# Performance work log

Hardware: AMD Instinct MI355X
Metric: run time of the kernel (lower is better)

## Reference

```python
import jax, jax.numpy as jnp
import numpy as np

B, H, M, K = 256, 1024, 20, 20  # batch, hidden, max_ingr, pairing top_k (must be equal: M==K)
VOCAB, INGR_V = 32000, 5000


def setup_inputs() -> dict:
    key = jax.random.key(0)
    ks = jax.random.split(key, 24)
    s = 0.02
    inp = {
        "input_ids": jax.random.randint(ks[0], (1, B), 0, VOCAB),
        "hidden": jax.random.normal(ks[1], (1, B, H), jnp.float32),
        "encoder_outputs": jax.random.normal(ks[2], (M, B, 2 * H), jnp.float32),
        "input_tensor": jax.random.randint(ks[3], (B, M), 0, INGR_V),
        "pairing_ids": jax.random.randint(ks[4], (INGR_V, K), 0, INGR_V),
        # parameters
        "emb_dec": jax.random.normal(ks[5], (VOCAB, H), jnp.float32) * s,
        "enc_emb": jax.random.normal(ks[6], (INGR_V, 2 * H), jnp.float32) * s,
        "Wq_i": jax.random.normal(ks[7], (H, H), jnp.float32) * s,
        "Wk_i": jax.random.normal(ks[8], (2 * H, H), jnp.float32) * s,
        "wa_i": jax.random.normal(ks[9], (H,), jnp.float32) * s,
        "Wq_p": jax.random.normal(ks[10], (H, H), jnp.float32) * s,
        "Wk_p": jax.random.normal(ks[11], (2 * H, H), jnp.float32) * s,
        "wa_p": jax.random.normal(ks[12], (H,), jnp.float32) * s,
        "ba_p": jax.random.normal(ks[13], (), jnp.float32) * s,
        "W_lin": jax.random.normal(ks[14], (3 * H, 2 * H), jnp.float32) * s,
        "b_lin": jnp.zeros((2 * H,), jnp.float32),
        "W_ih": jax.random.normal(ks[15], (3 * H, 2 * H), jnp.float32) * s,
        "W_hh": jax.random.normal(ks[16], (3 * H, H), jnp.float32) * s,
        "b_ih": jnp.zeros((3 * H,), jnp.float32),
        "b_hh": jnp.zeros((3 * H,), jnp.float32),
        "W_out": jax.random.normal(ks[17], (H, VOCAB), jnp.float32) * s,
        "b_out": jnp.zeros((VOCAB,), jnp.float32),
    }
    return inp


def reference(input_ids, hidden, encoder_outputs, input_tensor, pairing_ids,
              emb_dec, enc_emb, Wq_i, Wk_i, wa_i, Wq_p, Wk_p, wa_p, ba_p,
              W_lin, b_lin, W_ih, W_hh, b_ih, b_hh, W_out, b_out):
    h = hidden[0]                              # (B, H)
    emb = jnp.take(emb_dec, input_ids[0], axis=0)  # (B, H)

    # ---- IngrAtt (additive attention over ingredients) ----
    # torch code does a raw .view(B, M, 2H) on a (M, B, 2H) tensor -> plain reshape
    enc = encoder_outputs.reshape(B, M, 2 * H)
    query = h @ Wq_i                           # (B, H)
    key = enc @ Wk_i                           # (B, M, H)
    scores_i = jnp.tanh(query[:, None, :] + key) @ wa_i  # (B, M)
    aw = jax.nn.softmax(scores_i, axis=-1)     # (B, M)

    # ---- retrieval: pick most-attended ingredient, gather its top-k pairings ----
    ingr_arg = jnp.argmax(aw, axis=1)                          # (B,)
    ingr_id = input_tensor[jnp.arange(B), ingr_arg]            # (B,)
    comp_ids = jnp.take(pairing_ids, ingr_id, axis=0)          # (B, K)
    comp_emb = jnp.take(enc_emb, comp_ids, axis=0)             # (B, K, 2H)

    # ---- PairingAtt ----
    q_p = h @ Wq_p                             # (B, H)
    k_p = comp_emb @ Wk_p                      # (B, K, H)
    s_p = jnp.tanh(q_p[:, None, :] + k_p) @ wa_p + ba_p  # (B, K)
    a_p = jax.nn.softmax(s_p, axis=-1)
    attn_scores = a_p * s_p                    # (B, K) softmax-weighted raw scores
    attn_app = jnp.einsum('bk,bkd->bd', attn_scores, comp_emb)  # (B, 2H)

    out_pair = jnp.concatenate([emb, attn_app], axis=-1)  # (B, 3H)
    x = out_pair @ W_lin + b_lin                           # (B, 2H) -> GRU input

    # ---- single GRU step (torch gate ordering r,z,n) ----
    gi = x @ W_ih.T + b_ih
    gh = h @ W_hh.T + b_hh
    i_r, i_z, i_n = jnp.split(gi, 3, axis=-1)
    h_r, h_z, h_n = jnp.split(gh, 3, axis=-1)
    r = jax.nn.sigmoid(i_r + h_r)
    z = jax.nn.sigmoid(i_z + h_z)
    n = jnp.tanh(i_n + r * h_n)
    h_new = (1.0 - z) * n + z * h              # (B, H)

    logits = h_new @ W_out + b_out             # (B, VOCAB)
    return logits
```

## Files before the change

kernel.cpp:

```cpp
#include <hip/hip_runtime.h>
#include <cstdio>


using f32x4   = __attribute__((ext_vector_type(4))) float;
using bf16x8  = __attribute__((ext_vector_type(8))) short;
using ushort8 = __attribute__((ext_vector_type(8))) unsigned short;

__device__ __forceinline__ unsigned short f2bf(float x) {
    unsigned u = __builtin_bit_cast(unsigned, x);
    u += 0x7fffu + ((u >> 16) & 1u);
    return (unsigned short)(u >> 16);
}
__device__ __forceinline__ float bf2f(unsigned short u) {
    return __builtin_bit_cast(float, ((unsigned)u) << 16);
}

__device__ __forceinline__ void gload16(const void* g, void* l) {
    auto gp = (const __attribute__((address_space(1))) void*)g;
    auto lp = (__attribute__((address_space(3))) void*)l;
    __builtin_amdgcn_global_load_lds(gp, lp, 16, 0, 0);
}

__device__ __forceinline__ void transpose_body(
    const float* __restrict__ in, unsigned short* __restrict__ out,
    int R, int C, int r0, int c0)
{
    __shared__ float t[32][129];
    const int tid = threadIdx.x;
    const int lr = tid >> 3;
    const int cc = (tid & 7) * 4;
    #pragma unroll
    for (int i = 0; i < 4; ++i) {
        int r = lr + 32 * i;
        float4 v = *(const float4*)(in + (size_t)(r0 + r) * C + c0 + cc);
        t[cc + 0][r] = v.x; t[cc + 1][r] = v.y;
        t[cc + 2][r] = v.z; t[cc + 3][r] = v.w;
    }
    __syncthreads();
    const int rc = (tid & 15) * 8;
    #pragma unroll
    for (int p = 0; p < 2; ++p) {
        int c = (tid >> 4) + 16 * p;
        const float* src = &t[c][rc];
        ushort8 o;
        #pragma unroll
        for (int j = 0; j < 8; ++j) o[j] = f2bf(src[j]);
        *(ushort8*)(out + (size_t)(c0 + c) * R + r0 + rc) = o;
    }
}

__global__ __launch_bounds__(256) void prep1_kernel(
    const float* __restrict__ hidden, const float* __restrict__ enc_out,
    const float* __restrict__ enc_emb,
    const float* __restrict__ Wq_i, const float* __restrict__ Wq_p,
    const float* __restrict__ Wk_i, const float* __restrict__ Wk_p,
    unsigned short* __restrict__ hb, unsigned short* __restrict__ encb,
    unsigned short* __restrict__ encembb,
    unsigned short* __restrict__ WqiT, unsigned short* __restrict__ WqpT,
    unsigned short* __restrict__ WkiT, unsigned short* __restrict__ WkpT)
{
    const int bid = blockIdx.x;
    if (bid < 20496) {
        int i = bid * 256 + threadIdx.x;
        const float* src; unsigned short* dst; int j;
        if (i < 65536)        { src = hidden;  dst = hb;      j = i; }
        else if (i < 2686976) { src = enc_out; dst = encb;    j = i - 65536; }
        else                  { src = enc_emb; dst = encembb; j = i - 2686976; }
        float4 v = ((const float4*)src)[j];
        ((ushort4*)dst)[j] = make_ushort4(f2bf(v.x), f2bf(v.y), f2bf(v.z), f2bf(v.w));
    } else if (bid < 21008) {
        int local = bid - 20496;
        int bz = local >> 8, rem = local & 255;
        transpose_body(bz ? Wq_p : Wq_i, bz ? WqpT : WqiT,
                       1024, 1024, (rem >> 5) * 128, (rem & 31) * 32);
    } else {
        int local = bid - 21008;
        int bz = local >> 9, rem = local & 511;
        transpose_body(bz ? Wk_p : Wk_i, bz ? WkpT : WkiT,
                       2048, 1024, (rem >> 5) * 128, (rem & 31) * 32);
    }
}

template<int OUTBF, bool HAS_BIAS>
__device__ __forceinline__ void gemm_core(
    const unsigned short* __restrict__ A, const unsigned short* __restrict__ Bt,
    const float* __restrict__ bias, void* __restrict__ Cout, int Ncols,
    int sA, int sB, int kLen, int m0, int n0,
    unsigned short* lA, unsigned short* lB)
{
    const int tid = threadIdx.x;
    const int lane = tid & 63, wave = tid >> 6;
    const int wr = wave >> 1, wc = wave & 1;
    const int srow = tid >> 3, schunk = tid & 7;
    const int lm = lane & 15, lk = (lane >> 4) * 8;

    f32x4 acc[4][4];
    #pragma unroll
    for (int m = 0; m < 4; ++m)
        #pragma unroll
        for (int n = 0; n < 4; ++n) { f32x4 z = {0.f,0.f,0.f,0.f}; acc[m][n] = z; }

    const unsigned short* Ag = A  + (size_t)(m0 + srow) * sA + schunk * 8;
    const unsigned short* Bg = Bt + (size_t)(n0 + srow) * sB + schunk * 8;
    const int nt = kLen >> 6;

    char* lap = (char*)lA + tid * 16;
    char* lbp = (char*)lB + tid * 16;

    for (int t = 0; t < nt; ++t) {
        #pragma unroll
        for (int i = 0; i < 4; ++i) {
            gload16(Ag + (size_t)(32 * i) * sA + t * 64, lap + i * 4096);
            gload16(Bg + (size_t)(32 * i) * sB + t * 64, lbp + i * 4096);
        }
        __syncthreads();
        #pragma unroll
        for (int kk = 0; kk < 2; ++kk) {
            bf16x8 af[4], bv[4];
            #pragma unroll
            for (int m = 0; m < 4; ++m)
                af[m] = *(const bf16x8*)((const char*)lA +
                          (wr * 64 + m * 16 + lm) * 128 + (kk * 32 + lk) * 2);
            #pragma unroll
            for (int n = 0; n < 4; ++n)
                bv[n] = *(const bf16x8*)((const char*)lB +
                          (wc * 64 + n * 16 + lm) * 128 + (kk * 32 + lk) * 2);
            #pragma unroll
            for (int m = 0; m < 4; ++m)
                #pragma unroll
                for (int n = 0; n < 4; ++n)
                    acc[m][n] = __builtin_amdgcn_mfma_f32_16x16x32_bf16(
                        af[m], bv[n], acc[m][n], 0, 0, 0);
        }
        __syncthreads();
    }

    const int rbase = m0 + wr * 64 + (lane >> 4) * 4;
    const int cbase = n0 + wc * 64 + lm;
    #pragma unroll
    for (int m = 0; m < 4; ++m) {
        #pragma unroll
        for (int n = 0; n < 4; ++n) {
            int col = cbase + n * 16;
            float bvv = HAS_BIAS ? bias[col] : 0.0f;
            #pragma unroll
            for (int j = 0; j < 4; ++j) {
                int row = rbase + m * 16 + j;
                float v = acc[m][n][j] + bvv;
                if (OUTBF)
                    ((unsigned short*)Cout)[(size_t)row * Ncols + col] = f2bf(v);
                else
                    ((float*)Cout)[(size_t)row * Ncols + col] = v;
            }
        }
    }
}

#define GEMM_SHARED \
    __shared__ unsigned short lA[8192]; __shared__ unsigned short lB[8192];

__global__ __launch_bounds__(256) void gemm_dual_kernel(
    const unsigned short* A, const unsigned short* B0, const unsigned short* B1,
    float* P0, float* P1)
{
    GEMM_SHARED
    const int g = blockIdx.z >> 3, s = blockIdx.z & 7;
    const unsigned short* Bt = (g ? B1 : B0) + s * 128;
    float* C = (g ? P1 : P0) + (size_t)s * 262144;
    gemm_core<0,false>(A + s * 128, Bt, nullptr, C, 1024, 1024, 1024, 128,
                       blockIdx.y * 128, blockIdx.x * 128, lA, lB);
}

__global__ __launch_bounds__(256) void reduceq_kernel(
    const float* __restrict__ pqQ, const float* __restrict__ pqP,
    float* __restrict__ query, float* __restrict__ qp)
{
    int i = blockIdx.x * 256 + threadIdx.x;
    const float4* p; float4* o; int j;
    if (i < 65536) { p = (const float4*)pqQ; o = (float4*)query; j = i; }
    else           { p = (const float4*)pqP; o = (float4*)qp;    j = i - 65536; }
    float s0 = 0.f, s1 = 0.f, s2 = 0.f, s3 = 0.f;
    #pragma unroll
    for (int s = 0; s < 8; ++s) {
        float4 v = p[j + s * 65536];
        s0 += v.x; s1 += v.y; s2 += v.z; s3 += v.w;
    }
    o[j] = make_float4(s0, s1, s2, s3);
}

__global__ __launch_bounds__(256) void gemm24p_kernel(
    const unsigned short* encembb, const unsigned short* encb,
    const unsigned short* WkpT, const unsigned short* WkiT,
    unsigned short* kpP, unsigned short* keyP, size_t pStride)
{
    __shared__ unsigned short lA0[4096]; __shared__ unsigned short lA1[4096];
    __shared__ unsigned short lB0[4096]; __shared__ unsigned short lB1[4096];
    const int g = blockIdx.z >> 1, h = blockIdx.z & 1;
    const unsigned short* A  = (g ? encb : encembb) + h * 1024;
    const unsigned short* Bt = (g ? WkiT : WkpT)    + h * 1024;
    unsigned short* Cb = (g ? keyP : kpP) + (size_t)h * pStride;
    const int m0 = blockIdx.y * 128, n0 = blockIdx.x * 128;
    const int tid = threadIdx.x;
    const int lane = tid & 63, wave = tid >> 6;
    const int wr = wave >> 1, wc = wave & 1;
    const int lm = lane & 15;
    const int q  = lane >> 4;
    const int srow = tid >> 2;
    const int sc   = (tid & 3) ^ (srow & 3);

    f32x4 acc[4][4];
    #pragma unroll
    for (int m = 0; m < 4; ++m)
        #pragma unroll
        for (int n = 0; n < 4; ++n) { f32x4 z = {0.f,0.f,0.f,0.f}; acc[m][n] = z; }

    const unsigned short* Ag = A  + (size_t)(m0 + srow) * 2048 + sc * 8;
    const unsigned short* Bg = Bt + (size_t)(n0 + srow) * 2048 + sc * 8;

    auto stage = [&](unsigned short* la_, unsigned short* lb_, int t) {
        char* pa = (char*)la_ + tid * 16;
        char* pb = (char*)lb_ + tid * 16;
        gload16(Ag + t * 32, pa);
        gload16(Ag + (size_t)64 * 2048 + t * 32, pa + 4096);
        gload16(Bg + t * 32, pb);
        gload16(Bg + (size_t)64 * 2048 + t * 32, pb + 4096);
    };
    auto compute = [&](const unsigned short* la_, const unsigned short* lb_) {
        bf16x8 af[4], bv[4];
        #pragma unroll
        for (int m = 0; m < 4; ++m) {
            int r = wr * 64 + m * 16 + lm;
            af[m] = *(const bf16x8*)((const char*)la_ + r * 64 + ((q ^ (r & 3)) * 16));
        }
        #pragma unroll
        for (int n = 0; n < 4; ++n) {
            int r = wc * 64 + n * 16 + lm;
            bv[n] = *(const bf16x8*)((const char*)lb_ + r * 64 + ((q ^ (r & 3)) * 16));
        }
        #pragma unroll
        for (int m = 0; m < 4; ++m)
            #pragma unroll
            for (int n = 0; n < 4; ++n)
                acc[m][n] = __builtin_amdgcn_mfma_f32_16x16x32_bf16(
                    af[m], bv[n], acc[m][n], 0, 0, 0);
    };

    stage(lA0, lB0, 0);
    stage(lA1, lB1, 1);
    asm volatile("s_waitcnt vmcnt(4)" ::: "memory");
    __builtin_amdgcn_s_barrier();
    __builtin_amdgcn_sched_barrier(0);

    for (int t = 0; t < 30; t += 2) {
        compute(lA0, lB0);
        __builtin_amdgcn_s_barrier();
        __builtin_amdgcn_sched_barrier(0);
        stage(lA0, lB0, t + 2);
        asm volatile("s_waitcnt vmcnt(4)" ::: "memory");
        __builtin_amdgcn_s_barrier();
        __builtin_amdgcn_sched_barrier(0);

        compute(lA1, lB1);
        __builtin_amdgcn_s_barrier();
        __builtin_amdgcn_sched_barrier(0);
        stage(lA1, lB1, t + 3);
        asm volatile("s_waitcnt vmcnt(4)" ::: "memory");
        __builtin_amdgcn_s_barrier();
        __builtin_amdgcn_sched_barrier(0);
    }
    compute(lA0, lB0);
    asm volatile("s_waitcnt vmcnt(0)" ::: "memory");
    __builtin_amdgcn_s_barrier();
    __builtin_amdgcn_sched_barrier(0);
    compute(lA1, lB1);

    const int rbase = m0 + wr * 64 + q * 4;
    const int cbase = n0 + wc * 64 + lm;
    #pragma unroll
    for (int m = 0; m < 4; ++m)
        #pragma unroll
        for (int n = 0; n < 4; ++n)
            #pragma unroll
            for (int j = 0; j < 4; ++j)
                Cb[(size_t)(rbase + m * 16 + j) * 1024 + cbase + n * 16] =
                    f2bf(acc[m][n][j]);
}

__global__ __launch_bounds__(256) void attn_scores2_kernel(
    const float* __restrict__ q, const unsigned short* __restrict__ kP,
    size_t kStride, const float* __restrict__ wa, float* __restrict__ scores)
{
    const int bm = blockIdx.x;
    const int b  = bm / 20;
    const int tid = threadIdx.x;
    float4 qv  = ((const float4*)(q + (size_t)b * 1024))[tid];
    ushort4 k0 = ((const ushort4*)(kP + (size_t)bm * 1024))[tid];
    ushort4 k1 = ((const ushort4*)(kP + kStride + (size_t)bm * 1024))[tid];
    float4 wv  = ((const float4*)wa)[tid];
    float p = tanhf(qv.x + bf2f(k0.x) + bf2f(k1.x)) * wv.x
            + tanhf(qv.y + bf2f(k0.y) + bf2f(k1.y)) * wv.y
            + tanhf(qv.z + bf2f(k0.z) + bf2f(k1.z)) * wv.z
            + tanhf(qv.w + bf2f(k0.w) + bf2f(k1.w)) * wv.w;
    #pragma unroll
    for (int off = 32; off > 0; off >>= 1) p += __shfl_down(p, off);
    __shared__ float sp[4];
    if ((tid & 63) == 0) sp[tid >> 6] = p;
    __syncthreads();
    if (tid == 0) scores[bm] = sp[0] + sp[1] + sp[2] + sp[3];
}

__device__ __forceinline__ int argmax_ing(
    const float* __restrict__ sc_i, const int* __restrict__ input_tensor, int b)
{
    float best = sc_i[b * 20]; int bi = 0;
    #pragma unroll
    for (int m = 1; m < 20; ++m) {
        float v = sc_i[b * 20 + m];
        if (v > best) { best = v; bi = m; }
    }
    return input_tensor[b * 20 + bi];
}

__global__ __launch_bounds__(256) void attn_scores_gather2_kernel(
    const float* __restrict__ q, const unsigned short* __restrict__ kP,
    size_t kStride, const float* __restrict__ wa, const float* __restrict__ ba,
    const float* __restrict__ sc_i, const int* __restrict__ input_tensor,
    const int* __restrict__ pairing_ids, float* __restrict__ scores)
{
    const int bm = blockIdx.x;
    const int b  = bm / 20;
    const int kk = bm - b * 20;
    const int tid = threadIdx.x;
    const int ing = argmax_ing(sc_i, input_tensor, b);
    const int cid = pairing_ids[ing * 20 + kk];
    float4 qv  = ((const float4*)(q + (size_t)b * 1024))[tid];
    ushort4 k0 = ((const ushort4*)(kP + (size_t)cid * 1024))[tid];
    ushort4 k1 = ((const ushort4*)(kP + kStride + (size_t)cid * 1024))[tid];
    float4 wv  = ((const float4*)wa)[tid];
    float p = tanhf(qv.x + bf2f(k0.x) + bf2f(k1.x)) * wv.x
            + tanhf(qv.y + bf2f(k0.y) + bf2f(k1.y)) * wv.y
            + tanhf(qv.z + bf2f(k0.z) + bf2f(k1.z)) * wv.z
            + tanhf(qv.w + bf2f(k0.w) + bf2f(k1.w)) * wv.w;
    #pragma unroll
    for (int off = 32; off > 0; off >>= 1) p += __shfl_down(p, off);
    __shared__ float sp[4];
    if ((tid & 63) == 0) sp[tid >> 6] = p;
    __syncthreads();
    if (tid == 0) scores[bm] = sp[0] + sp[1] + sp[2] + sp[3] + ba[0];
}

__global__ __launch_bounds__(256) void out_pair_kernel(
    const float* __restrict__ s_p, const float* __restrict__ enc_emb,
    const float* __restrict__ sc_i, const int* __restrict__ input_tensor,
    const int* __restrict__ pairing_ids,
    const float* __restrict__ emb_dec, const int* __restrict__ input_ids,
    unsigned short* __restrict__ out_pairb)
{
    const int b = blockIdx.x / 6, seg = blockIdx.x % 6;
    const int tid = threadIdx.x;
    const int d = seg * 512 + tid * 2;
    ushort2 o;
    if (seg < 2) {
        float2 v = *(const float2*)(emb_dec + (size_t)input_ids[b] * 1024 + d);
        o.x = f2bf(v.x); o.y = f2bf(v.y);
    } else {
        const int ing = argmax_ing(sc_i, input_tensor, b);
        __shared__ float s_raw[20];
        if (tid < 20) s_raw[tid] = s_p[b * 20 + tid];
        __syncthreads();
        float mx = -1e30f;
        #pragma unroll
        for (int m = 0; m < 20; ++m) mx = fmaxf(mx, s_raw[m]);
        float den = 0.f; float w[20];
        #pragma unroll
        for (int m = 0; m < 20; ++m) { w[m] = expf(s_raw[m] - mx); den += w[m]; }
        const float inv = 1.f / den;
        const int dd = d - 1024;
        float a0 = 0.f, a1 = 0.f;
        #pragma unroll
        for (int k = 0; k < 20; ++k) {
            const int cid = pairing_ids[ing * 20 + k];
            float2 v = *(const float2*)(enc_emb + (size_t)cid * 2048 + dd);
            float a = w[k] * inv * s_raw[k];
            a0 += a * v.x; a1 += a * v.y;
        }
        o.x = f2bf(a0); o.y = f2bf(a1);
    }
    *(ushort2*)(out_pairb + (size_t)b * 3072 + d) = o;
}

__global__ __launch_bounds__(256) void gemm5f_kernel(
    const unsigned short* __restrict__ A, const float* __restrict__ Wlin,
    float* __restrict__ P)
{
    __shared__ unsigned short lA[8192];
    __shared__ unsigned short lB[8192];
    const int tid = threadIdx.x;
    const int lane = tid & 63, wave = tid >> 6;
    const int wr = wave >> 1, wc = wave & 1;
    const int m0 = blockIdx.y * 128, n0 = blockIdx.x * 128;
    const int koff = blockIdx.z * 192;
    const int srow = tid >> 3, schunk = tid & 7;
    const int lm = lane & 15, lk = (lane >> 4) * 8;
    const int bcol = tid & 127, bkg = tid >> 7;
    const int bsw  = (bcol & 7) << 4;

    f32x4 acc[4][4];
    #pragma unroll
    for (int m = 0; m < 4; ++m)
        #pragma unroll
        for (int n = 0; n < 4; ++n) { f32x4 z = {0.f,0.f,0.f,0.f}; acc[m][n] = z; }

    const unsigned short* Ag = A + (size_t)(m0 + srow) * 3072 + koff + schunk * 8;
    char* lap = (char*)lA + tid * 16;

    for (int t = 0; t < 3; ++t) {
        #pragma unroll
        for (int i = 0; i < 4; ++i)
            gload16(Ag + (size_t)(32 * i) * 3072 + t * 64, lap + i * 4096);
        #pragma unroll
        for (int hh = 0; hh < 2; ++hh) {
            const int kbase = koff + t * 64 + bkg * 32 + hh * 16;
            ushort8 o0, o1;
            #pragma unroll
            for (int j = 0; j < 8; ++j)
                o0[j] = f2bf(Wlin[(size_t)(kbase + j) * 2048 + n0 + bcol]);
            #pragma unroll
            for (int j = 0; j < 8; ++j)
                o1[j] = f2bf(Wlin[(size_t)(kbase + 8 + j) * 2048 + n0 + bcol]);
            char* base = (char*)lB + bcol * 128;
            *(ushort8*)(base + ((bkg * 64 + hh * 32)      ^ bsw)) = o0;
            *(ushort8*)(base + ((bkg * 64 + hh * 32 + 16) ^ bsw)) = o1;
        }
        __syncthreads();
        #pragma unroll
        for (int kk = 0; kk < 2; ++kk) {
            bf16x8 af[4], bv[4];
            #pragma unroll
            for (int m = 0; m < 4; ++m)
                af[m] = *(const bf16x8*)((const char*)lA +
                          (wr * 64 + m * 16 + lm) * 128 + (kk * 32 + lk) * 2);
            #pragma unroll
            for (int n = 0; n < 4; ++n) {
                int rr = wc * 64 + n * 16 + lm;
                bv[n] = *(const bf16x8*)((const char*)lB +
                          rr * 128 + (((kk * 32 + lk) * 2) ^ ((rr & 7) << 4)));
            }
            #pragma unroll
            for (int m = 0; m < 4; ++m)
                #pragma unroll
                for (int n = 0; n < 4; ++n)
                    acc[m][n] = __builtin_amdgcn_mfma_f32_16x16x32_bf16(
                        af[m], bv[n], acc[m][n], 0, 0, 0);
        }
        __syncthreads();
    }

    float* C = P + (size_t)blockIdx.z * 524288;
    const int rbase = m0 + wr * 64 + (lane >> 4) * 4;
    const int cbase = n0 + wc * 64 + lm;
    #pragma unroll
    for (int m = 0; m < 4; ++m)
        #pragma unroll
        for (int n = 0; n < 4; ++n)
            #pragma unroll
            for (int j = 0; j < 4; ++j)
                C[(size_t)(rbase + m * 16 + j) * 2048 + cbase + n * 16] = acc[m][n][j];
}

__global__ __launch_bounds__(256) void gemm67f_kernel(
    const unsigned short* __restrict__ xb, const unsigned short* __restrict__ hb,
    const float* __restrict__ Wih, const float* __restrict__ Whh,
    float* __restrict__ pg)
{
    __shared__ unsigned short lA[8192];
    __shared__ unsigned short lB[8192];
    const int tid = threadIdx.x;
    const int lane = tid & 63, wave = tid >> 6;
    const int wr = wave >> 1, wc = wave & 1;
    const int g = blockIdx.z >> 2, s = blockIdx.z & 3;
    const unsigned short* A = g ? hb : xb;
    const float* Bf = g ? Whh : Wih;
    const int sA   = g ? 1024 : 2048;
    const int koff = g ? s * 256 : s * 512;
    const int nt   = g ? 4 : 8;
    const int m0 = blockIdx.y * 128, n0 = blockIdx.x * 128;
    const int srow = tid >> 3, schunk = tid & 7;
    const int lm = lane & 15, lk = (lane >> 4) * 8;
    const int bsw = (srow & 7) << 4;

    f32x4 acc[4][4];
    #pragma unroll
    for (int m = 0; m < 4; ++m)
        #pragma unroll
        for (int n = 0; n < 4; ++n) { f32x4 z = {0.f,0.f,0.f,0.f}; acc[m][n] = z; }

    const unsigned short* Ag = A  + (size_t)(m0 + srow) * sA + koff + schunk * 8;
    const float*          Bg = Bf + (size_t)(n0 + srow) * sA + koff + schunk * 8;
    char* lap = (char*)lA + tid * 16;

    for (int t = 0; t < nt; ++t) {
        #pragma unroll
        for (int i = 0; i < 4; ++i)
            gload16(Ag + (size_t)(32 * i) * sA + t * 64, lap + i * 4096);
        #pragma unroll
        for (int i = 0; i < 4; ++i) {
            const float* src = Bg + (size_t)(32 * i) * sA + t * 64;
            float4 v0 = *(const float4*)(src);
            float4 v1 = *(const float4*)(src + 4);
            ushort8 o;
            o[0] = f2bf(v0.x); o[1] = f2bf(v0.y); o[2] = f2bf(v0.z); o[3] = f2bf(v0.w);
            o[4] = f2bf(v1.x); o[5] = f2bf(v1.y); o[6] = f2bf(v1.z); o[7] = f2bf(v1.w);
            *(ushort8*)((char*)lB + (srow + 32 * i) * 128 + ((schunk * 16) ^ bsw)) = o;
        }
        __syncthreads();
        #pragma unroll
        for (int kk = 0; kk < 2; ++kk) {
            bf16x8 af[4], bv[4];
            #pragma unroll
            for (int m = 0; m < 4; ++m)
                af[m] = *(const bf16x8*)((const char*)lA +
                          (wr * 64 + m * 16 + lm) * 128 + (kk * 32 + lk) * 2);
            #pragma unroll
            for (int n = 0; n < 4; ++n) {
                int rr = wc * 64 + n * 16 + lm;
                bv[n] = *(const bf16x8*)((const char*)lB +
                          rr * 128 + (((kk * 32 + lk) * 2) ^ ((rr & 7) << 4)));
            }
            #pragma unroll
            for (int m = 0; m < 4; ++m)
                #pragma unroll
                for (int n = 0; n < 4; ++n)
                    acc[m][n] = __builtin_amdgcn_mfma_f32_16x16x32_bf16(
                        af[m], bv[n], acc[m][n], 0, 0, 0);
        }
        __syncthreads();
    }

    float* C = pg + (size_t)blockIdx.z * 786432;
    const int rbase = m0 + wr * 64 + (lane >> 4) * 4;
    const int cbase = n0 + wc * 64 + lm;
    #pragma unroll
    for (int m = 0; m < 4; ++m)
        #pragma unroll
        for (int n = 0; n < 4; ++n)
            #pragma unroll
            for (int j = 0; j < 4; ++j)
                C[(size_t)(rbase + m * 16 + j) * 3072 + cbase + n * 16] = acc[m][n][j];
}

__global__ __launch_bounds__(256) void gemm8_kernel(
    const unsigned short* __restrict__ A, const float* __restrict__ Wout,
    const float* __restrict__ bias, float* __restrict__ C)
{
    __shared__ unsigned short lA0[16384]; __shared__ unsigned short lA1[16384];
    __shared__ unsigned short lB0[4096];  __shared__ unsigned short lB1[4096];
    const int tid  = threadIdx.x;
    const int lane = tid & 63, wave = tid >> 6;
    const int n0 = blockIdx.x * 64;
    const int lm = lane & 15, lk = (lane >> 4) * 8;
    const int srow = tid >> 3, schunk = tid & 7;
    const int bcol = tid & 63, bkg = tid >> 6;
    const int bsw  = (bcol & 7) << 4;

    f32x4 acc[4][4];
    #pragma unroll
    for (int m = 0; m < 4; ++m)
        #pragma unroll
        for (int n = 0; n < 4; ++n) { f32x4 z = {0.f,0.f,0.f,0.f}; acc[m][n] = z; }

    const unsigned short* Ag = A + (size_t)srow * 1024 + schunk * 8;

    auto stageA = [&](unsigned short* la_, int t) {
        char* la = (char*)la_ + tid * 16;
        #pragma unroll
        for (int i = 0; i < 8; ++i)
            gload16(Ag + (size_t)(32 * i) * 1024 + t * 64, la + i * 4096);
    };
    float bv_[16];
    auto loadB = [&](int t) {
        const float* src = Wout + (size_t)(t * 64 + bkg * 16) * 32000 + n0 + bcol;
        #pragma unroll
        for (int j = 0; j < 16; ++j) bv_[j] = src[(size_t)j * 32000];
    };
    auto writeB = [&](unsigned short* lb_) {
        ushort8 o0, o1;
        #pragma unroll
        for (int j = 0; j < 8; ++j) { o0[j] = f2bf(bv_[j]); o1[j] = f2bf(bv_[j + 8]); }
        char* base = (char*)lb_ + bcol * 128;
        *(ushort8*)(base + ((bkg * 32)      ^ bsw)) = o0;
        *(ushort8*)(base + ((bkg * 32 + 16) ^ bsw)) = o1;
    };
    auto compute = [&](const unsigned short* la_, const unsigned short* lb_) {
        #pragma unroll
        for (int kk = 0; kk < 2; ++kk) {
            bf16x8 af[4], bv[4];
            #pragma unroll
            for (int m = 0; m < 4; ++m)
                af[m] = *(const bf16x8*)((const char*)la_ +
                          (wave * 64 + m * 16 + lm) * 128 + (kk * 32 + lk) * 2);
            #pragma unroll
            for (int n = 0; n < 4; ++n) {
                int rr = n * 16 + lm;
                bv[n] = *(const bf16x8*)((const char*)lb_ +
                          rr * 128 + (((kk * 32 + lk) * 2) ^ ((rr & 7) << 4)));
            }
            #pragma unroll
            for (int m = 0; m < 4; ++m)
                #pragma unroll
                for (int n = 0; n < 4; ++n)
                    acc[m][n] = __builtin_amdgcn_mfma_f32_16x16x32_bf16(
                        af[m], bv[n], acc[m][n], 0, 0, 0);
        }
    };

    stageA(lA0, 0); loadB(0); writeB(lB0);
    __syncthreads();
    const int nt = 16;
    for (int t = 0; t < nt; t += 2) {
        if (t + 1 < nt) { stageA(lA1, t + 1); loadB(t + 1); }
        compute(lA0, lB0);
        if (t + 1 < nt) writeB(lB1);
        __syncthreads();
        if (t + 1 < nt) {
            if (t + 2 < nt) { stageA(lA0, t + 2); loadB(t + 2); }
            compute(lA1, lB1);
            if (t + 2 < nt) writeB(lB0);
            __syncthreads();
        }
    }

    const int rbase = wave * 64 + (lane >> 4) * 4;
    const int cbase = n0 + lm;
    #pragma unroll
    for (int m = 0; m < 4; ++m) {
        #pragma unroll
        for (int n = 0; n < 4; ++n) {
            int col = cbase + n * 16;
            float bvv = bias[col];
            #pragma unroll
            for (int j = 0; j < 4; ++j)
                C[(size_t)(rbase + m * 16 + j) * 32000 + col] = acc[m][n][j] + bvv;
        }
    }
}

__global__ __launch_bounds__(256) void reduce5_kernel(
    const float* __restrict__ P, const float* __restrict__ bias,
    unsigned short* __restrict__ xb)
{
    int i = blockIdx.x * 256 + threadIdx.x;
    const float4* p = (const float4*)P;
    float4 bb = ((const float4*)bias)[i & 511];
    float s0 = bb.x, s1 = bb.y, s2 = bb.z, s3 = bb.w;
    #pragma unroll
    for (int s = 0; s < 16; ++s) {
        float4 v = p[i + s * 131072];
        s0 += v.x; s1 += v.y; s2 += v.z; s3 += v.w;
    }
    ((ushort4*)xb)[i] = make_ushort4(f2bf(s0), f2bf(s1), f2bf(s2), f2bf(s3));
}

__global__ __launch_bounds__(256) void gru_kernel(
    const float* __restrict__ pg, const float* __restrict__ b_ih,
    const float* __restrict__ b_hh, const float* __restrict__ h,
    unsigned short* __restrict__ hnewb)
{
    int idx = blockIdx.x * 256 + threadIdx.x;
    int b = idx >> 10, j = idx & 1023;
    float ir = b_ih[j], iz = b_ih[1024 + j], in_ = b_ih[2048 + j];
    float hr = b_hh[j], hz = b_hh[1024 + j], hn  = b_hh[2048 + j];
    #pragma unroll
    for (int s = 0; s < 4; ++s) {
        const float* gi = pg + (size_t)s * 786432 + (size_t)b * 3072;
        ir  += gi[j]; iz += gi[1024 + j]; in_ += gi[2048 + j];
        const float* gh = pg + (size_t)(4 + s) * 786432 + (size_t)b * 3072;
        hr  += gh[j]; hz += gh[1024 + j]; hn  += gh[2048 + j];
    }
    float r = 1.f / (1.f + expf(-(ir + hr)));
    float z = 1.f / (1.f + expf(-(iz + hz)));
    float n = tanhf(in_ + r * hn);
    hnewb[idx] = f2bf((1.f - z) * n + z * h[idx]);
}

extern "C" void kernel_launch(void* const* d_in, const int* in_sizes, int n_in,
                              void* d_out, int out_size, void* d_ws, size_t ws_size,
                              hipStream_t stream)
{
    const int*   input_ids    = (const int*)  d_in[0];
    const float* hidden       = (const float*)d_in[1];
    const float* enc_out      = (const float*)d_in[2];
    const int*   input_tensor = (const int*)  d_in[3];
    const int*   pairing_ids  = (const int*)  d_in[4];
    const float* emb_dec      = (const float*)d_in[5];
    const float* enc_emb      = (const float*)d_in[6];
    const float* Wq_i  = (const float*)d_in[7];
    const float* Wk_i  = (const float*)d_in[8];
    const float* wa_i  = (const float*)d_in[9];
    const float* Wq_p  = (const float*)d_in[10];
    const float* Wk_p  = (const float*)d_in[11];
    const float* wa_p  = (const float*)d_in[12];
    const float* ba_p  = (const float*)d_in[13];
    const float* W_lin = (const float*)d_in[14];
    const float* b_lin = (const float*)d_in[15];
    const float* W_ih  = (const float*)d_in[16];
    const float* W_hh  = (const float*)d_in[17];
    const float* b_ih  = (const float*)d_in[18];
    const float* b_hh  = (const float*)d_in[19];
    const float* W_out = (const float*)d_in[20];
    const float* b_out = (const float*)d_in[21];

    constexpr size_t OFF_HB    = 0;
    constexpr size_t OFF_HNEW  = 524288;
    constexpr size_t OFF_WQI   = 1048576;
    constexpr size_t OFF_WQP   = 3145728;
    constexpr size_t OFF_WKI   = 5242880;
    constexpr size_t OFF_WKP   = 9437184;
    constexpr size_t OFF_ENC   = 13631488;
    constexpr size_t OFF_SLOT1 = 34603008;
    constexpr size_t OFF_SLOT2 = 55574528;
    constexpr size_t OFF_QUERY = 76546048;
    constexpr size_t OFF_QP    = 77594624;
    constexpr size_t OFF_SCI   = 78643200;
    constexpr size_t OFF_SCP   = 78667776;
    constexpr size_t OFF_PGI   = 1048576;
    constexpr size_t NEED      = 79167488;
    if (ws_size < NEED) {
        fprintf(stderr, "kernel_launch: ws_size %zu < needed %zu\n", ws_size, NEED);
        return;
    }
    char* ws = (char*)d_ws;
    unsigned short* hb     = (unsigned short*)(ws + OFF_HB);
    unsigned short* hnewb  = (unsigned short*)(ws + OFF_HNEW);
    unsigned short* WqiT   = (unsigned short*)(ws + OFF_WQI);
    unsigned short* WqpT   = (unsigned short*)(ws + OFF_WQP);
    unsigned short* WkiT   = (unsigned short*)(ws + OFF_WKI);
    unsigned short* WkpT   = (unsigned short*)(ws + OFF_WKP);
    unsigned short* encb   = (unsigned short*)(ws + OFF_ENC);
    float*          pqQ    = (float*)         (ws + OFF_SLOT1);
    float*          pqP    = (float*)         (ws + OFF_SLOT1 + 8388608);
    unsigned short* kpP    = (unsigned short*)(ws + OFF_SLOT1);
    unsigned short* encembb= (unsigned short*)(ws + OFF_SLOT2);
    unsigned short* outp   = (unsigned short*)(ws + OFF_SLOT1);
    unsigned short* xb     = (unsigned short*)(ws + OFF_SLOT1 + 18350080);
    float*          query  = (float*)         (ws + OFF_QUERY);
    float*          qp     = (float*)         (ws + OFF_QP);
    float*          sc_i   = (float*)         (ws + OFF_SCI);
    float*          sc_p   = (float*)         (ws + OFF_SCP);
    float*          pgi    = (float*)         (ws + OFF_PGI);
    unsigned short* keyP   = (unsigned short*)d_out;
    float*          pG5    = (float*)d_out;

    constexpr size_t KP_STRIDE = 5120 * 1024;

    prep1_kernel<<<22032, 256, 0, stream>>>(hidden, enc_out, enc_emb,
                                            Wq_i, Wq_p, Wk_i, Wk_p,
                                            hb, encb, encembb,
                                            WqiT, WqpT, WkiT, WkpT);

    gemm_dual_kernel<<<dim3(8, 2, 16), 256, 0, stream>>>(hb, WqiT, WqpT, pqQ, pqP);
    reduceq_kernel<<<512, 256, 0, stream>>>(pqQ, pqP, query, qp);

    gemm24p_kernel<<<dim3(8, 40, 4), 256, 0, stream>>>(encembb, encb, WkpT, WkiT,
                                                       kpP, keyP, KP_STRIDE);

    attn_scores2_kernel<<<5120, 256, 0, stream>>>(query, keyP, KP_STRIDE, wa_i, sc_i);
    attn_scores_gather2_kernel<<<5120, 256, 0, stream>>>(qp, kpP, KP_STRIDE, wa_p, ba_p,
                                                         sc_i, input_tensor, pairing_ids, sc_p);

    out_pair_kernel<<<1536, 256, 0, stream>>>(sc_p, enc_emb, sc_i, input_tensor,
                                              pairing_ids, emb_dec, input_ids, outp);

    gemm5f_kernel<<<dim3(16, 2, 16), 256, 0, stream>>>(outp, W_lin, pG5);
    reduce5_kernel<<<512, 256, 0, stream>>>(pG5, b_lin, xb);

    gemm67f_kernel<<<dim3(24, 2, 8), 256, 0, stream>>>(xb, hb, W_ih, W_hh, pgi);

    gru_kernel<<<1024, 256, 0, stream>>>(pgi, b_ih, b_hh, hidden, hnewb);

    gemm8_kernel<<<500, 256, 0, stream>>>(hnewb, W_out, b_out, (float*)d_out);
}
```

Measured before the change: 224.6 us.

## Fold split-K query reduction into attention score kernels and remap gemm24p blocks per XCD

The query split-K GEMM now uses 4 K-slices instead of 8, and the separate reduceq kernel is removed. The attention score kernels sum the four partial query vectors themselves when they load q. The gemm24p launch becomes a 1D grid whose block index is remapped so each XCD works on a contiguous group of tiles from one sub-problem, aiming for better L2 reuse. The trade-offs are one fewer launch and less partial traffic, but each of the 5120 score blocks now does four redundant partial loads, and the partials are moved into spare space in the output buffer.

After: 220.5 us, median of 2. About the same (-1.8%).

```diff
diff --git a/kernel.cpp b/kernel.cpp
--- a/kernel.cpp
+++ b/kernel.cpp
@@ -164,28 +164,11 @@
     float* P0, float* P1)
 {
     GEMM_SHARED
-    const int g = blockIdx.z >> 3, s = blockIdx.z & 7;
-    const unsigned short* Bt = (g ? B1 : B0) + s * 128;
+    const int g = blockIdx.z >> 2, s = blockIdx.z & 3;
+    const unsigned short* Bt = (g ? B1 : B0) + s * 256;
     float* C = (g ? P1 : P0) + (size_t)s * 262144;
-    gemm_core<0,false>(A + s * 128, Bt, nullptr, C, 1024, 1024, 1024, 128,
+    gemm_core<0,false>(A + s * 256, Bt, nullptr, C, 1024, 1024, 1024, 256,
                        blockIdx.y * 128, blockIdx.x * 128, lA, lB);
-}
-
-__global__ __launch_bounds__(256) void reduceq_kernel(
-    const float* __restrict__ pqQ, const float* __restrict__ pqP,
-    float* __restrict__ query, float* __restrict__ qp)
-{
-    int i = blockIdx.x * 256 + threadIdx.x;
-    const float4* p; float4* o; int j;
-    if (i < 65536) { p = (const float4*)pqQ; o = (float4*)query; j = i; }
-    else           { p = (const float4*)pqP; o = (float4*)qp;    j = i - 65536; }
-    float s0 = 0.f, s1 = 0.f, s2 = 0.f, s3 = 0.f;
-    #pragma unroll
-    for (int s = 0; s < 8; ++s) {
-        float4 v = p[j + s * 65536];
-        s0 += v.x; s1 += v.y; s2 += v.z; s3 += v.w;
-    }
-    o[j] = make_float4(s0, s1, s2, s3);
 }
 
 __global__ __launch_bounds__(256) void gemm24p_kernel(
@@ -195,11 +178,17 @@
 {
     __shared__ unsigned short lA0[4096]; __shared__ unsigned short lA1[4096];
     __shared__ unsigned short lB0[4096]; __shared__ unsigned short lB1[4096];
-    const int g = blockIdx.z >> 1, h = blockIdx.z & 1;
+    const int w   = (int)blockIdx.x;
+    const int xcd = w & 7;
+    const int r   = w >> 3;
+    const int z   = xcd >> 1;
+    const int by  = (xcd & 1) * 20 + (r >> 3);
+    const int bx  = r & 7;
+    const int g = z >> 1, h = z & 1;
     const unsigned short* A  = (g ? encb : encembb) + h * 1024;
     const unsigned short* Bt = (g ? WkiT : WkpT)    + h * 1024;
     unsigned short* Cb = (g ? keyP : kpP) + (size_t)h * pStride;
-    const int m0 = blockIdx.y * 128, n0 = blockIdx.x * 128;
+    const int m0 = by * 128, n0 = bx * 128;
     const int tid = threadIdx.x;
     const int lane = tid & 63, wave = tid >> 6;
     const int wr = wave >> 1, wc = wave & 1;
@@ -212,7 +201,7 @@
     #pragma unroll
     for (int m = 0; m < 4; ++m)
         #pragma unroll
-        for (int n = 0; n < 4; ++n) { f32x4 z = {0.f,0.f,0.f,0.f}; acc[m][n] = z; }
+        for (int n = 0; n < 4; ++n) { f32x4 zz = {0.f,0.f,0.f,0.f}; acc[m][n] = zz; }
 
     const unsigned short* Ag = A  + (size_t)(m0 + srow) * 2048 + sc * 8;
     const unsigned short* Bg = Bt + (size_t)(n0 + srow) * 2048 + sc * 8;
@@ -229,13 +218,13 @@
         bf16x8 af[4], bv[4];
         #pragma unroll
         for (int m = 0; m < 4; ++m) {
-            int r = wr * 64 + m * 16 + lm;
-            af[m] = *(const bf16x8*)((const char*)la_ + r * 64 + ((q ^ (r & 3)) * 16));
+            int rr = wr * 64 + m * 16 + lm;
+            af[m] = *(const bf16x8*)((const char*)la_ + rr * 64 + ((q ^ (rr & 3)) * 16));
         }
         #pragma unroll
         for (int n = 0; n < 4; ++n) {
-            int r = wc * 64 + n * 16 + lm;
-            bv[n] = *(const bf16x8*)((const char*)lb_ + r * 64 + ((q ^ (r & 3)) * 16));
+            int rr = wc * 64 + n * 16 + lm;
+            bv[n] = *(const bf16x8*)((const char*)lb_ + rr * 64 + ((q ^ (rr & 3)) * 16));
         }
         #pragma unroll
         for (int m = 0; m < 4; ++m)
@@ -286,14 +275,19 @@
                     f2bf(acc[m][n][j]);
 }
 
-__global__ __launch_bounds__(256) void attn_scores2_kernel(
-    const float* __restrict__ q, const unsigned short* __restrict__ kP,
+__global__ __launch_bounds__(256) void attn_scores2q_kernel(
+    const float* __restrict__ pqQ, const unsigned short* __restrict__ kP,
     size_t kStride, const float* __restrict__ wa, float* __restrict__ scores)
 {
     const int bm = blockIdx.x;
     const int b  = bm / 20;
     const int tid = threadIdx.x;
-    float4 qv  = ((const float4*)(q + (size_t)b * 1024))[tid];
+    float4 qa = ((const float4*)(pqQ + (size_t)b * 1024))[tid];
+    float4 qb = ((const float4*)(pqQ + 262144 + (size_t)b * 1024))[tid];
+    float4 qc = ((const float4*)(pqQ + 524288 + (size_t)b * 1024))[tid];
+    float4 qd = ((const float4*)(pqQ + 786432 + (size_t)b * 1024))[tid];
+    float4 qv = make_float4(qa.x + qb.x + qc.x + qd.x, qa.y + qb.y + qc.y + qd.y,
+                            qa.z + qb.z + qc.z + qd.z, qa.w + qb.w + qc.w + qd.w);
     ushort4 k0 = ((const ushort4*)(kP + (size_t)bm * 1024))[tid];
     ushort4 k1 = ((const ushort4*)(kP + kStride + (size_t)bm * 1024))[tid];
     float4 wv  = ((const float4*)wa)[tid];
@@ -321,8 +315,8 @@
     return input_tensor[b * 20 + bi];
 }
 
-__global__ __launch_bounds__(256) void attn_scores_gather2_kernel(
-    const float* __restrict__ q, const unsigned short* __restrict__ kP,
+__global__ __launch_bounds__(256) void attn_scores_gather2q_kernel(
+    const float* __restrict__ pqP, const unsigned short* __restrict__ kP,
     size_t kStride, const float* __restrict__ wa, const float* __restrict__ ba,
     const float* __restrict__ sc_i, const int* __restrict__ input_tensor,
     const int* __restrict__ pairing_ids, float* __restrict__ scores)
@@ -333,7 +327,12 @@
     const int tid = threadIdx.x;
     const int ing = argmax_ing(sc_i, input_tensor, b);
     const int cid = pairing_ids[ing * 20 + kk];
-    float4 qv  = ((const float4*)(q + (size_t)b * 1024))[tid];
+    float4 qa = ((const float4*)(pqP + (size_t)b * 1024))[tid];
+    float4 qb = ((const float4*)(pqP + 262144 + (size_t)b * 1024))[tid];
+    float4 qc = ((const float4*)(pqP + 524288 + (size_t)b * 1024))[tid];
+    float4 qd = ((const float4*)(pqP + 786432 + (size_t)b * 1024))[tid];
+    float4 qv = make_float4(qa.x + qb.x + qc.x + qd.x, qa.y + qb.y + qc.y + qd.y,
+                            qa.z + qb.z + qc.z + qd.z, qa.w + qb.w + qc.w + qd.w);
     ushort4 k0 = ((const ushort4*)(kP + (size_t)cid * 1024))[tid];
     ushort4 k1 = ((const ushort4*)(kP + kStride + (size_t)cid * 1024))[tid];
     float4 wv  = ((const float4*)wa)[tid];
@@ -719,8 +718,6 @@
     constexpr size_t OFF_ENC   = 13631488;
     constexpr size_t OFF_SLOT1 = 34603008;
     constexpr size_t OFF_SLOT2 = 55574528;
-    constexpr size_t OFF_QUERY = 76546048;
-    constexpr size_t OFF_QP    = 77594624;
     constexpr size_t OFF_SCI   = 78643200;
     constexpr size_t OFF_SCP   = 78667776;
     constexpr size_t OFF_PGI   = 1048576;
@@ -737,18 +734,16 @@
     unsigned short* WkiT   = (unsigned short*)(ws + OFF_WKI);
     unsigned short* WkpT   = (unsigned short*)(ws + OFF_WKP);
     unsigned short* encb   = (unsigned short*)(ws + OFF_ENC);
-    float*          pqQ    = (float*)         (ws + OFF_SLOT1);
-    float*          pqP    = (float*)         (ws + OFF_SLOT1 + 8388608);
     unsigned short* kpP    = (unsigned short*)(ws + OFF_SLOT1);
     unsigned short* encembb= (unsigned short*)(ws + OFF_SLOT2);
     unsigned short* outp   = (unsigned short*)(ws + OFF_SLOT1);
     unsigned short* xb     = (unsigned short*)(ws + OFF_SLOT1 + 18350080);
-    float*          query  = (float*)         (ws + OFF_QUERY);
-    float*          qp     = (float*)         (ws + OFF_QP);
     float*          sc_i   = (float*)         (ws + OFF_SCI);
     float*          sc_p   = (float*)         (ws + OFF_SCP);
     float*          pgi    = (float*)         (ws + OFF_PGI);
     unsigned short* keyP   = (unsigned short*)d_out;
+    float*          pqQ    = (float*)((char*)d_out + 20971520);
+    float*          pqP    = (float*)((char*)d_out + 20971520 + 4194304);
     float*          pG5    = (float*)d_out;
 
     constexpr size_t KP_STRIDE = 5120 * 1024;
@@ -758,15 +753,14 @@
                                             hb, encb, encembb,
                                             WqiT, WqpT, WkiT, WkpT);
 
-    gemm_dual_kernel<<<dim3(8, 2, 16), 256, 0, stream>>>(hb, WqiT, WqpT, pqQ, pqP);
-    reduceq_kernel<<<512, 256, 0, stream>>>(pqQ, pqP, query, qp);
-
-    gemm24p_kernel<<<dim3(8, 40, 4), 256, 0, stream>>>(encembb, encb, WkpT, WkiT,
-                                                       kpP, keyP, KP_STRIDE);
-
-    attn_scores2_kernel<<<5120, 256, 0, stream>>>(query, keyP, KP_STRIDE, wa_i, sc_i);
-    attn_scores_gather2_kernel<<<5120, 256, 0, stream>>>(qp, kpP, KP_STRIDE, wa_p, ba_p,
-                                                         sc_i, input_tensor, pairing_ids, sc_p);
+    gemm_dual_kernel<<<dim3(8, 2, 8), 256, 0, stream>>>(hb, WqiT, WqpT, pqQ, pqP);
+
+    gemm24p_kernel<<<1280, 256, 0, stream>>>(encembb, encb, WkpT, WkiT,
+                                             kpP, keyP, KP_STRIDE);
+
+    attn_scores2q_kernel<<<5120, 256, 0, stream>>>(pqQ, keyP, KP_STRIDE, wa_i, sc_i);
+    attn_scores_gather2q_kernel<<<5120, 256, 0, stream>>>(pqP, kpP, KP_STRIDE, wa_p, ba_p,
+                                                          sc_i, input_tensor, pairing_ids, sc_p);
 
     out_pair_kernel<<<1536, 256, 0, stream>>>(sc_p, enc_emb, sc_i, input_tensor,
                                               pairing_ids, emb_dec, input_ids, outp);
```
